# Kernel optimization log

Hardware: AMD Instinct MI355X
Metric: run time of the kernel (lower is better)

The kernel has to match this reference:

```python
import jax, jax.numpy as jnp
import numpy as np

B, D_IN, D, E = 65536, 512, 512, 8  # batch, input dim, node hidden dim, n_children (=decision dim)


def setup_inputs() -> dict:
    key = jax.random.key(0)
    ks = jax.random.split(key, 5)
    s = 0.02  # weight init scale
    return {
        "x": jax.random.normal(ks[0], (B, D_IN), jnp.float32),
        "W_root": jax.random.normal(ks[1], (D_IN, D), jnp.float32) * s,
        "b_root": jnp.zeros((D,), jnp.float32),
        "W_dec": jax.random.normal(ks[2], (D, E), jnp.float32) * s,
        "b_dec": jnp.zeros((E,), jnp.float32),
        "W_leaf": jax.random.normal(ks[3], (E, D, D), jnp.float32) * s,
        "b_leaf": jnp.zeros((E, D), jnp.float32),
        "W_ldec": jax.random.normal(ks[4], (E, D, E), jnp.float32) * s,
        "b_ldec": jnp.zeros((E, E), jnp.float32),
    }


def reference(x, W_root, b_root, W_dec, b_dec, W_leaf, b_leaf, W_ldec, b_ldec):
    # Root node (Dense+relu), flatten is a no-op on [B, D]
    h = jax.nn.relu(x @ W_root + b_root)                                 # [B, D]
    dec = jax.nn.softmax(h @ W_dec + b_dec, axis=-1)                     # [B, E] root decision (softmax, outputDim>1)
    route = jnp.argmax(dec, axis=-1)                                     # [B] hard routing
    # Leaf children: each leaf applies its own node Dense+relu and decision Dense+softmax.
    # Dense reference for the boolean-mask dispatch/combine: compute all experts on all
    # samples, then gather each sample's routed expert output (math-equivalent to the
    # original gather-per-mask + concat + reorder-gather, since partitions are disjoint).
    lh = jax.nn.relu(jnp.einsum('bd,edh->ebh', h, W_leaf) + b_leaf[:, None, :])     # [E, B, D]
    ldec = jax.nn.softmax(jnp.einsum('ebd,edo->ebo', lh, W_ldec) + b_ldec[:, None, :], axis=-1)  # [E, B, E]
    sel = jnp.take_along_axis(ldec.transpose(1, 0, 2), route[:, None, None], axis=1)[:, 0]  # [B, E]
    # concat root decisionOut [B,1,E] with ordered leaf outputs [B,1,E] along axis -2
    return jnp.concatenate([dec[:, None, :], sel[:, None, :]], axis=1)  # [B, 2, E]
```

## Files before the change

### kernel.cpp

```cpp
#include <hip/hip_runtime.h>
#include <stdint.h>

#define DD   512
#define EE   8

typedef __bf16 bf16x8 __attribute__((ext_vector_type(8)));
typedef float  f32x4  __attribute__((ext_vector_type(4)));

__device__ __forceinline__ unsigned short f2bf(float f) {
    union { float f; unsigned int i; } v; v.f = f;
    unsigned int x = v.i;
    x += 0x7fffu + ((x >> 16) & 1u);
    return (unsigned short)(x >> 16);
}
__device__ __forceinline__ void gload_lds16(const void* g, void* l) {
    __builtin_amdgcn_global_load_lds(
        (const __attribute__((address_space(1))) unsigned int*)g,
        (__attribute__((address_space(3))) unsigned int*)l, 16, 0, 0);
}
__device__ __forceinline__ f32x4 mfma_bf16(bf16x8 a, bf16x8 b, f32x4 c) {
    return __builtin_amdgcn_mfma_f32_16x16x32_bf16(a, b, c, 0, 0, 0);
}

__global__ __launch_bounds__(256) void k_wsplit(
    const float* __restrict__ W_root,
    unsigned short* __restrict__ WrTh, unsigned short* __restrict__ WrTl)
{
    __shared__ float tile[64][65];
    int tl = blockIdx.x, tr = tl >> 3, tc = tl & 7;
    int t = threadIdx.x;
    #pragma unroll
    for (int j = 0; j < 16; j++) {
        int i2 = t + j * 256; int r = i2 >> 6, c = i2 & 63;
        tile[r][c] = W_root[(size_t)(tr * 64 + r) * DD + tc * 64 + c];
    }
    __syncthreads();
    #pragma unroll
    for (int j = 0; j < 16; j++) {
        int i2 = t + j * 256; int r = i2 >> 6, c = i2 & 63;
        float v = tile[c][r];
        __bf16 hb = (__bf16)v;
        __bf16 lb = (__bf16)(v - (float)hb);
        size_t di = (size_t)(tc * 64 + r) * DD + tr * 64 + c;
        union { __bf16 b; unsigned short u; } uh, ul; uh.b = hb; ul.b = lb;
        WrTh[di] = uh.u; WrTl[di] = ul.u;
    }
}

__global__ __launch_bounds__(256) void k_trW(
    const float* __restrict__ W_leaf, unsigned short* __restrict__ WlT)
{
    __shared__ unsigned short tile[64][65];
    int bid = blockIdx.x;
    int e = bid >> 6;
    int tl = bid & 63, tr = tl >> 3, tc = tl & 7;
    const float* src = W_leaf + (size_t)e * DD * DD;
    unsigned short* dst = WlT + (size_t)e * DD * DD;
    int t = threadIdx.x;
    #pragma unroll
    for (int j = 0; j < 16; j++) {
        int i2 = t + j * 256; int r = i2 >> 6, c = i2 & 63;
        tile[r][c] = f2bf(src[(size_t)(tr * 64 + r) * DD + tc * 64 + c]);
    }
    __syncthreads();
    #pragma unroll
    for (int j = 0; j < 16; j++) {
        int i2 = t + j * 256; int r = i2 >> 6, c = i2 & 63;
        dst[(size_t)(tc * 64 + r) * DD + tr * 64 + c] = tile[c][r];
    }
}

__global__ __launch_bounds__(256) void k_trpad(
    const float* __restrict__ W_ldec, unsigned short* __restrict__ WldT)
{
    int idx = blockIdx.x * 256 + threadIdx.x;
    int e = idx >> 13, rem = idx & 8191;
    int o = rem >> 9, k = rem & 511;
    unsigned short v = 0;
    if (o < 8) v = f2bf(W_ldec[((size_t)e * DD + k) * EE + o]);
    WldT[idx] = v;
}

__global__ __launch_bounds__(256) void k_root(
    const float* __restrict__ x,
    const unsigned short* __restrict__ WrTh,
    const unsigned short* __restrict__ WrTl,
    const float* __restrict__ b_root,
    const float* __restrict__ W_dec,
    unsigned short* __restrict__ hbuf,
    float* __restrict__ logit_part)
{
    __shared__ unsigned short lsAh[128 * 32];
    __shared__ unsigned short lsAl[128 * 32];
    __shared__ unsigned short lsBh[128 * 32];
    __shared__ unsigned short lsBl[128 * 32];

    int bid = blockIdx.x;
    int mb = (bid >> 5) * 8 + (bid & 7);
    int cb = (bid >> 3) & 3;
    int m0 = mb * 128, n0 = cb * 128;

    int t = threadIdx.x;
    int wid = t >> 6, lane = t & 63;
    int wr = wid >> 1, wc = wid & 1;
    int l15 = lane & 15, l4 = lane >> 4;

    int ar = t >> 1, ah16 = (t & 1) * 16;
    const float* pA = x + (size_t)(m0 + ar) * DD + ah16;
    const unsigned short* srcBh0 = WrTh + (size_t)(n0 + (t >> 2)) * DD + (t & 3) * 8;
    const unsigned short* srcBh1 = srcBh0 + (size_t)64 * DD;
    const unsigned short* srcBl0 = WrTl + (size_t)(n0 + (t >> 2)) * DD + (t & 3) * 8;
    const unsigned short* srcBl1 = srcBl0 + (size_t)64 * DD;
    unsigned short* dBh0 = &lsBh[t * 8];
    unsigned short* dBh1 = &lsBh[2048 + t * 8];
    unsigned short* dBl0 = &lsBl[t * 8];
    unsigned short* dBl1 = &lsBl[2048 + t * 8];

    f32x4 acc[4][4];
    #pragma unroll
    for (int m = 0; m < 4; m++)
        #pragma unroll
        for (int n = 0; n < 4; n++) acc[m][n] = (f32x4){0.f, 0.f, 0.f, 0.f};

    for (int k0 = 0; k0 < DD; k0 += 32) {
        const float4* pAv = (const float4*)(pA + k0);
        float4 v0 = pAv[0], v1 = pAv[1], v2 = pAv[2], v3 = pAv[3];
        float vv[16] = {v0.x,v0.y,v0.z,v0.w, v1.x,v1.y,v1.z,v1.w,
                        v2.x,v2.y,v2.z,v2.w, v3.x,v3.y,v3.z,v3.w};
        bf16x8 hv0, hv1, lv0, lv1;
        #pragma unroll
        for (int j = 0; j < 8; j++) {
            __bf16 hb = (__bf16)vv[j];
            hv0[j] = hb; lv0[j] = (__bf16)(vv[j] - (float)hb);
        }
        #pragma unroll
        for (int j = 0; j < 8; j++) {
            __bf16 hb = (__bf16)vv[8 + j];
            hv1[j] = hb; lv1[j] = (__bf16)(vv[8 + j] - (float)hb);
        }
        __syncthreads();
        *(bf16x8*)&lsAh[ar * 32 + ah16]     = hv0;
        *(bf16x8*)&lsAh[ar * 32 + ah16 + 8] = hv1;
        *(bf16x8*)&lsAl[ar * 32 + ah16]     = lv0;
        *(bf16x8*)&lsAl[ar * 32 + ah16 + 8] = lv1;
        gload_lds16(srcBh0 + k0, dBh0);
        gload_lds16(srcBh1 + k0, dBh1);
        gload_lds16(srcBl0 + k0, dBl0);
        gload_lds16(srcBl1 + k0, dBl1);
        __syncthreads();

        bf16x8 fah[4], fal[4], fbh[4], fbl[4];
        #pragma unroll
        for (int m = 0; m < 4; m++) {
            int ro = (wr * 64 + m * 16 + l15) * 32 + l4 * 8;
            fah[m] = *(const bf16x8*)&lsAh[ro];
            fal[m] = *(const bf16x8*)&lsAl[ro];
        }
        #pragma unroll
        for (int n = 0; n < 4; n++) {
            int ro = (wc * 64 + n * 16 + l15) * 32 + l4 * 8;
            fbh[n] = *(const bf16x8*)&lsBh[ro];
            fbl[n] = *(const bf16x8*)&lsBl[ro];
        }
        #pragma unroll
        for (int m = 0; m < 4; m++)
            #pragma unroll
            for (int n = 0; n < 4; n++) {
                acc[m][n] = mfma_bf16(fah[m], fbh[n], acc[m][n]);
                acc[m][n] = mfma_bf16(fah[m], fbl[n], acc[m][n]);
                acc[m][n] = mfma_bf16(fal[m], fbh[n], acc[m][n]);
            }
    }

    float wdl[4][8], bcol[4];
    #pragma unroll
    for (int n = 0; n < 4; n++) {
        int colg = n0 + wc * 64 + n * 16 + l15;
        bcol[n] = b_root[colg];
        #pragma unroll
        for (int o = 0; o < 8; o++) wdl[n][o] = W_dec[colg * 8 + o];
    }
    int p = cb * 2 + wc;
    #pragma unroll
    for (int m = 0; m < 4; m++) {
        #pragma unroll
        for (int i = 0; i < 4; i++) {
            int rowg = m0 + wr * 64 + m * 16 + l4 * 4 + i;
            float s[8];
            #pragma unroll
            for (int o = 0; o < 8; o++) s[o] = 0.f;
            #pragma unroll
            for (int n = 0; n < 4; n++) {
                float v = acc[m][n][i] + bcol[n];
                v = fmaxf(v, 0.f);
                hbuf[(size_t)rowg * DD + (n0 + wc * 64 + n * 16 + l15)] = f2bf(v);
                #pragma unroll
                for (int o = 0; o < 8; o++) s[o] = fmaf(v, wdl[n][o], s[o]);
            }
            #pragma unroll
            for (int d = 1; d < 16; d <<= 1)
                #pragma unroll
                for (int o = 0; o < 8; o++) s[o] += __shfl_xor(s[o], d, 64);
            if (l15 == 0) {
                #pragma unroll
                for (int o = 0; o < 8; o++)
                    logit_part[((size_t)p * 65536 + rowg) * 8 + o] = s[o];
            }
        }
    }
}

__global__ __launch_bounds__(256) void k_dec(
    const float* __restrict__ logit_part,
    const float* __restrict__ b_dec,
    float* __restrict__ out,
    int* __restrict__ route,
    int* __restrict__ meta,
    int* __restrict__ rescue_list)
{
    int b = blockIdx.x * 256 + threadIdx.x;
    double lg[8];
    #pragma unroll
    for (int o = 0; o < 8; o++) lg[o] = (double)b_dec[o];
    for (int ppp = 0; ppp < 8; ppp++) {
        #pragma unroll
        for (int o = 0; o < 8; o++)
            lg[o] += (double)logit_part[((size_t)ppp * 65536 + b) * 8 + o];
    }
    double mx = -1e300, mx2 = -1e300; int idx = 0;
    #pragma unroll
    for (int o = 0; o < 8; o++) {
        if (lg[o] > mx) { mx2 = mx; mx = lg[o]; idx = o; }
        else if (lg[o] > mx2) mx2 = lg[o];
    }
    double ev[8], s = 0.0;
    #pragma unroll
    for (int o = 0; o < 8; o++) { ev[o] = exp(lg[o] - mx); s += ev[o]; }
    double inv = 1.0 / s;
    float4 o0, o1;
    o0.x = (float)(ev[0]*inv); o0.y = (float)(ev[1]*inv);
    o0.z = (float)(ev[2]*inv); o0.w = (float)(ev[3]*inv);
    o1.x = (float)(ev[4]*inv); o1.y = (float)(ev[5]*inv);
    o1.z = (float)(ev[6]*inv); o1.w = (float)(ev[7]*inv);
    float4* op = (float4*)(out + (size_t)b * 16);
    op[0] = o0; op[1] = o1;
    route[b] = idx;
    if (mx - mx2 < 1e-4) {
        int pos = atomicAdd(&meta[27], 1);
        if (pos < 8192) rescue_list[pos] = b;
    }
}

__global__ __launch_bounds__(256) void k_rescue(
    const float* __restrict__ x,
    const float* __restrict__ W_root,
    const float* __restrict__ b_root,
    const float* __restrict__ W_dec,
    const float* __restrict__ b_dec,
    const int* __restrict__ rescue_list,
    const int* __restrict__ meta,
    float* __restrict__ out,
    int* __restrict__ route)
{
    int nresc = min(meta[27], 8192);
    if ((int)blockIdx.x >= nresc) return;
    int row = rescue_list[blockIdx.x];
    int t = threadIdx.x;

    __shared__ float xr[512];
    __shared__ double red[4][8];
    xr[t * 2]     = x[(size_t)row * DD + t * 2];
    xr[t * 2 + 1] = x[(size_t)row * DD + t * 2 + 1];
    __syncthreads();

    int d0 = t, d1 = t + 256;
    double a0 = 0.0, a1 = 0.0;
    for (int k = 0; k < DD; k++) {
        double xv = (double)xr[k];
        a0 += xv * (double)W_root[(size_t)k * DD + d0];
        a1 += xv * (double)W_root[(size_t)k * DD + d1];
    }
    double h0 = fmax(a0 + (double)b_root[d0], 0.0);
    double h1 = fmax(a1 + (double)b_root[d1], 0.0);
    double so[8];
    #pragma unroll
    for (int o = 0; o < 8; o++)
        so[o] = h0 * (double)W_dec[d0 * 8 + o] + h1 * (double)W_dec[d1 * 8 + o];
    #pragma unroll
    for (int d = 1; d < 64; d <<= 1)
        #pragma unroll
        for (int o = 0; o < 8; o++) so[o] += __shfl_xor(so[o], d, 64);
    if ((t & 63) == 0) {
        #pragma unroll
        for (int o = 0; o < 8; o++) red[t >> 6][o] = so[o];
    }
    __syncthreads();
    if (t == 0) {
        double lg[8]; double mx = -1e300; int idx = 0;
        #pragma unroll
        for (int o = 0; o < 8; o++) {
            lg[o] = red[0][o] + red[1][o] + red[2][o] + red[3][o] + (double)b_dec[o];
            if (lg[o] > mx) { mx = lg[o]; idx = o; }
        }
        double ev[8], s = 0.0;
        #pragma unroll
        for (int o = 0; o < 8; o++) { ev[o] = exp(lg[o] - mx); s += ev[o]; }
        double inv = 1.0 / s;
        float4 o0, o1;
        o0.x = (float)(ev[0]*inv); o0.y = (float)(ev[1]*inv);
        o0.z = (float)(ev[2]*inv); o0.w = (float)(ev[3]*inv);
        o1.x = (float)(ev[4]*inv); o1.y = (float)(ev[5]*inv);
        o1.z = (float)(ev[6]*inv); o1.w = (float)(ev[7]*inv);
        float4* op = (float4*)(out + (size_t)row * 16);
        op[0] = o0; op[1] = o1;
        route[row] = idx;
    }
}

__global__ __launch_bounds__(256) void k_count(
    const int* __restrict__ route, int* __restrict__ meta)
{
    __shared__ int wcnt[4][8];
    int b = blockIdx.x * 256 + threadIdx.x;
    int e = route[b];
    int lane = threadIdx.x & 63, wv = threadIdx.x >> 6;
    #pragma unroll
    for (int ex = 0; ex < 8; ex++) {
        unsigned long long m = __ballot(e == ex);
        if (lane == 0) wcnt[wv][ex] = __popcll(m);
    }
    __syncthreads();
    if (threadIdx.x < 8) {
        int ex = threadIdx.x;
        atomicAdd(&meta[ex], wcnt[0][ex] + wcnt[1][ex] + wcnt[2][ex] + wcnt[3][ex]);
    }
}

__global__ void k_scan(int* __restrict__ meta)
{
    if (threadIdx.x == 0 && blockIdx.x == 0) {
        int run = 0, rb = 0;
        for (int e = 0; e < 8; e++) {
            int c = meta[e];
            meta[16 + e] = run;
            meta[8 + e]  = run;
            int n = (c + 127) >> 7;
            for (int j = 0; j < n; j++) meta[32 + rb + j] = e | (j << 8);
            rb += n;
            run += n << 7;
        }
        meta[24] = rb;
    }
}

__global__ __launch_bounds__(256) void k_scatter(
    const int* __restrict__ route, int* __restrict__ meta, int* __restrict__ rows_list)
{
    __shared__ int wcnt[4][8];
    __shared__ int wbase[4][8];
    int b = blockIdx.x * 256 + threadIdx.x;
    int e = route[b];
    int lane = threadIdx.x & 63, wv = threadIdx.x >> 6;
    unsigned long long mymask = 0;
    #pragma unroll
    for (int ex = 0; ex < 8; ex++) {
        unsigned long long m = __ballot(e == ex);
        if (e == ex) mymask = m;
        if (lane == 0) wcnt[wv][ex] = __popcll(m);
    }
    int myrank = __popcll(mymask & ((1ULL << lane) - 1ULL));
    __syncthreads();
    if (threadIdx.x < 8) {
        int ex = threadIdx.x;
        int c0 = wcnt[0][ex], c1 = wcnt[1][ex], c2 = wcnt[2][ex], c3 = wcnt[3][ex];
        int base = atomicAdd(&meta[8 + ex], c0 + c1 + c2 + c3);
        wbase[0][ex] = base;
        wbase[1][ex] = base + c0;
        wbase[2][ex] = base + c0 + c1;
        wbase[3][ex] = base + c0 + c1 + c2;
    }
    __syncthreads();
    rows_list[wbase[wv][e] + myrank] = b;
}

__global__ __launch_bounds__(256) void k_gemm2(
    const unsigned short* __restrict__ hbuf,
    const unsigned short* __restrict__ WlT,
    const float* __restrict__ b_leaf,
    const unsigned short* __restrict__ WldT,
    const int* __restrict__ rows_list,
    const int* __restrict__ meta,
    float* __restrict__ ldec_part)
{
    __shared__ unsigned short lsA[128 * 32];
    __shared__ unsigned short lsB[128 * 32];
    __shared__ unsigned short lh[128 * 136];

    int bid = blockIdx.x;
    int rbid = (bid >> 5) * 8 + (bid & 7);
    int cb = (bid >> 3) & 3;
    if (rbid >= meta[24]) return;
    int pk = meta[32 + rbid];
    int e = pk & 255, lrb = pk >> 8;
    int poff_e = meta[16 + e], cnt_e = meta[e];
    int n0 = cb * 128;

    int t = threadIdx.x;
    int wid = t >> 6, lane = t & 63;
    int wr = wid >> 1, wc = wid & 1;
    int l15 = lane & 15, l4 = lane >> 4;

    int slot0 = poff_e + lrb * 128 + (t >> 2);
    int slot1 = slot0 + 64;
    int lastv = poff_e + cnt_e - 1;
    int grow0 = rows_list[min(slot0, lastv)];
    int grow1 = rows_list[min(slot1, lastv)];
    const unsigned short* srcA0 = hbuf + (size_t)grow0 * DD + (t & 3) * 8;
    const unsigned short* srcA1 = hbuf + (size_t)grow1 * DD + (t & 3) * 8;
    const unsigned short* srcB0 = WlT + (size_t)e * DD * DD + (size_t)(n0 + (t >> 2)) * DD + (t & 3) * 8;
    const unsigned short* srcB1 = srcB0 + (size_t)64 * DD;
    unsigned short* dA0 = &lsA[t * 8];
    unsigned short* dA1 = &lsA[2048 + t * 8];
    unsigned short* dB0 = &lsB[t * 8];
    unsigned short* dB1 = &lsB[2048 + t * 8];

    f32x4 acc[4][4];
    #pragma unroll
    for (int m = 0; m < 4; m++)
        #pragma unroll
        for (int n = 0; n < 4; n++) acc[m][n] = (f32x4){0.f, 0.f, 0.f, 0.f};

    for (int k0 = 0; k0 < DD; k0 += 32) {
        __syncthreads();
        gload_lds16(srcA0 + k0, dA0);
        gload_lds16(srcA1 + k0, dA1);
        gload_lds16(srcB0 + k0, dB0);
        gload_lds16(srcB1 + k0, dB1);
        __syncthreads();
        bf16x8 af[4], bfr[4];
        #pragma unroll
        for (int m = 0; m < 4; m++)
            af[m] = *(const bf16x8*)&lsA[(wr * 64 + m * 16 + l15) * 32 + l4 * 8];
        #pragma unroll
        for (int n = 0; n < 4; n++)
            bfr[n] = *(const bf16x8*)&lsB[(wc * 64 + n * 16 + l15) * 32 + l4 * 8];
        #pragma unroll
        for (int m = 0; m < 4; m++)
            #pragma unroll
            for (int n = 0; n < 4; n++)
                acc[m][n] = mfma_bf16(af[m], bfr[n], acc[m][n]);
    }

    #pragma unroll
    for (int n = 0; n < 4; n++) {
        int coll = wc * 64 + n * 16 + l15;
        float bv = b_leaf[(size_t)e * DD + n0 + coll];
        #pragma unroll
        for (int m = 0; m < 4; m++) {
            int rl = wr * 64 + m * 16 + l4 * 4;
            #pragma unroll
            for (int i = 0; i < 4; i++) {
                float v = acc[m][n][i] + bv;
                v = v > 0.f ? v : 0.f;
                lh[(rl + i) * 136 + coll] = f2bf(v);
            }
        }
    }
    __syncthreads();

    f32x4 acc2[2];
    acc2[0] = (f32x4){0.f, 0.f, 0.f, 0.f};
    acc2[1] = (f32x4){0.f, 0.f, 0.f, 0.f};
    #pragma unroll
    for (int kk = 0; kk < 4; kk++) {
        bf16x8 bb = *(const bf16x8*)(WldT + ((size_t)e * 16 + l15) * DD + n0 + kk * 32 + l4 * 8);
        #pragma unroll
        for (int m2 = 0; m2 < 2; m2++) {
            bf16x8 aa = *(const bf16x8*)&lh[(wid * 32 + m2 * 16 + l15) * 136 + kk * 32 + l4 * 8];
            acc2[m2] = mfma_bf16(aa, bb, acc2[m2]);
        }
    }
    if (l15 < 8) {
        #pragma unroll
        for (int m2 = 0; m2 < 2; m2++)
            #pragma unroll
            for (int i = 0; i < 4; i++) {
                int rl = wid * 32 + m2 * 16 + l4 * 4 + i;
                int s = min(poff_e + lrb * 128 + rl, lastv);
                int brow = rows_list[s];
                ldec_part[((size_t)cb * 65536 + brow) * 8 + l15] = acc2[m2][i];
            }
    }
}

__global__ __launch_bounds__(256) void k_sel(
    const float* __restrict__ ldec_part,
    const int* __restrict__ route,
    const float* __restrict__ b_ldec,
    float* __restrict__ out)
{
    int b = blockIdx.x * 256 + threadIdx.x;
    int e = route[b];
    float lg[8];
    #pragma unroll
    for (int o = 0; o < 8; o++) lg[o] = b_ldec[e * 8 + o];
    #pragma unroll
    for (int p = 0; p < 4; p++) {
        const float4* ap = (const float4*)(ldec_part + ((size_t)p * 65536 + b) * 8);
        float4 a0 = ap[0], a1 = ap[1];
        lg[0]+=a0.x; lg[1]+=a0.y; lg[2]+=a0.z; lg[3]+=a0.w;
        lg[4]+=a1.x; lg[5]+=a1.y; lg[6]+=a1.z; lg[7]+=a1.w;
    }
    float mx = -1e30f;
    #pragma unroll
    for (int o = 0; o < 8; o++) mx = fmaxf(mx, lg[o]);
    float ev[8], s = 0.f;
    #pragma unroll
    for (int o = 0; o < 8; o++) { ev[o] = expf(lg[o] - mx); s += ev[o]; }
    float inv = 1.f / s;
    float4 o0, o1;
    o0.x = ev[0]*inv; o0.y = ev[1]*inv; o0.z = ev[2]*inv; o0.w = ev[3]*inv;
    o1.x = ev[4]*inv; o1.y = ev[5]*inv; o1.z = ev[6]*inv; o1.w = ev[7]*inv;
    float4* op = (float4*)(out + (size_t)b * 16 + 8);
    op[0] = o0; op[1] = o1;
}

extern "C" void kernel_launch(void* const* d_in, const int* in_sizes, int n_in,
                              void* d_out, int out_size, void* d_ws, size_t ws_size,
                              hipStream_t stream)
{
    const float* x      = (const float*)d_in[0];
    const float* W_root = (const float*)d_in[1];
    const float* b_root = (const float*)d_in[2];
    const float* W_dec  = (const float*)d_in[3];
    const float* b_dec  = (const float*)d_in[4];
    const float* W_leaf = (const float*)d_in[5];
    const float* b_leaf = (const float*)d_in[6];
    const float* W_ldec = (const float*)d_in[7];
    const float* b_ldec = (const float*)d_in[8];
    float* out = (float*)d_out;

    char* w = (char*)d_ws;
    unsigned short* hbuf       = (unsigned short*)(w);
    float*          logit_part = (float*)(w + 67108864);
    unsigned short* WlT        = (unsigned short*)(w + 83886080);
    unsigned short* WldT       = (unsigned short*)(w + 88080384);
    float*          ldec_part  = (float*)(w + 88211456);
    int*            route      = (int*)(w + 96600064);
    int*            rows_list  = (int*)(w + 96862208);
    int*            meta       = (int*)(w + 97128448);
    unsigned short* WrTh       = (unsigned short*)(w + 97132544);
    unsigned short* WrTl       = (unsigned short*)(w + 97656832);
    int*            rescue     = (int*)(w + 98181120);
    const size_t WS_NEED = 98213888ULL;
    if (ws_size < WS_NEED) return;

    hipMemsetAsync(meta, 0, 4096, stream);

    k_wsplit <<<64,   256, 0, stream>>>(W_root, WrTh, WrTl);
    k_trW    <<<512,  256, 0, stream>>>(W_leaf, WlT);
    k_trpad  <<<256,  256, 0, stream>>>(W_ldec, WldT);
    k_root   <<<2048, 256, 0, stream>>>(x, WrTh, WrTl, b_root, W_dec, hbuf, logit_part);
    k_dec    <<<256,  256, 0, stream>>>(logit_part, b_dec, out, route, meta, rescue);
    k_rescue <<<8192, 256, 0, stream>>>(x, W_root, b_root, W_dec, b_dec, rescue, meta, out, route);
    k_count  <<<256,  256, 0, stream>>>(route, meta);
    k_scan   <<<1,    64,  0, stream>>>(meta);
    k_scatter<<<256,  256, 0, stream>>>(route, meta, rows_list);
    k_gemm2  <<<2080, 256, 0, stream>>>(hbuf, WlT, b_leaf, WldT, rows_list, meta, ldec_part);
    k_sel    <<<256,  256, 0, stream>>>(ldec_part, route, b_ldec, out);
}
```

Before: 290.2 us.

## Drop split-bf16 root GEMM, compute root logits via MFMA from staged LDS tile

The root GEMM now runs as a single bf16 MFMA pass instead of three hi/lo compensated passes, and the W_root low-part buffer is removed. To offset the lost precision, the near-tie rescue threshold is widened so more ambiguous rows get recomputed in fp32 by the rescue kernel. The epilogue stages the relu'd bf16 tile in LDS, writes hbuf with coalesced vector stores, and computes the decision logits with a small MFMA against a transposed padded W_dec. This replaces the per-lane FMA and shuffle reduction, and halves the logit partials from 8 to 4. Softmax in k_dec moves from double to float exp. Routing correctness now leans more on the rescue path, and the rescue count is capped at 8192.

```diff
diff --git a/kernel.cpp b/kernel.cpp
--- a/kernel.cpp
+++ b/kernel.cpp
@@ -6,6 +6,7 @@
 
 typedef __bf16 bf16x8 __attribute__((ext_vector_type(8)));
 typedef float  f32x4  __attribute__((ext_vector_type(4)));
+typedef unsigned short u16x8 __attribute__((ext_vector_type(8)));
 
 __device__ __forceinline__ unsigned short f2bf(float f) {
     union { float f; unsigned int i; } v; v.f = f;
@@ -22,28 +23,22 @@
     return __builtin_amdgcn_mfma_f32_16x16x32_bf16(a, b, c, 0, 0, 0);
 }
 
-__global__ __launch_bounds__(256) void k_wsplit(
-    const float* __restrict__ W_root,
-    unsigned short* __restrict__ WrTh, unsigned short* __restrict__ WrTl)
-{
-    __shared__ float tile[64][65];
+__global__ __launch_bounds__(256) void k_wtr(
+    const float* __restrict__ W_root, unsigned short* __restrict__ WrTh)
+{
+    __shared__ unsigned short tile[64][65];
     int tl = blockIdx.x, tr = tl >> 3, tc = tl & 7;
     int t = threadIdx.x;
     #pragma unroll
     for (int j = 0; j < 16; j++) {
         int i2 = t + j * 256; int r = i2 >> 6, c = i2 & 63;
-        tile[r][c] = W_root[(size_t)(tr * 64 + r) * DD + tc * 64 + c];
+        tile[r][c] = f2bf(W_root[(size_t)(tr * 64 + r) * DD + tc * 64 + c]);
     }
     __syncthreads();
     #pragma unroll
     for (int j = 0; j < 16; j++) {
         int i2 = t + j * 256; int r = i2 >> 6, c = i2 & 63;
-        float v = tile[c][r];
-        __bf16 hb = (__bf16)v;
-        __bf16 lb = (__bf16)(v - (float)hb);
-        size_t di = (size_t)(tc * 64 + r) * DD + tr * 64 + c;
-        union { __bf16 b; unsigned short u; } uh, ul; uh.b = hb; ul.b = lb;
-        WrTh[di] = uh.u; WrTl[di] = ul.u;
+        WrTh[(size_t)(tc * 64 + r) * DD + tr * 64 + c] = tile[c][r];
     }
 }
 
@@ -81,19 +76,25 @@
     WldT[idx] = v;
 }
 
+__global__ __launch_bounds__(256) void k_trdec(
+    const float* __restrict__ W_dec, unsigned short* __restrict__ WdT)
+{
+    int idx = blockIdx.x * 256 + threadIdx.x;
+    int o = idx >> 9, k = idx & 511;
+    WdT[idx] = (o < 8) ? f2bf(W_dec[(size_t)k * EE + o]) : (unsigned short)0;
+}
+
 __global__ __launch_bounds__(256) void k_root(
     const float* __restrict__ x,
     const unsigned short* __restrict__ WrTh,
-    const unsigned short* __restrict__ WrTl,
     const float* __restrict__ b_root,
-    const float* __restrict__ W_dec,
+    const unsigned short* __restrict__ WdT,
     unsigned short* __restrict__ hbuf,
     float* __restrict__ logit_part)
 {
-    __shared__ unsigned short lsAh[128 * 32];
-    __shared__ unsigned short lsAl[128 * 32];
-    __shared__ unsigned short lsBh[128 * 32];
-    __shared__ unsigned short lsBl[128 * 32];
+    __shared__ unsigned short smem[128 * 136];
+    unsigned short* lsA = smem;
+    unsigned short* lsB = smem + 4096;
 
     int bid = blockIdx.x;
     int mb = (bid >> 5) * 8 + (bid & 7);
@@ -107,14 +108,10 @@
 
     int ar = t >> 1, ah16 = (t & 1) * 16;
     const float* pA = x + (size_t)(m0 + ar) * DD + ah16;
-    const unsigned short* srcBh0 = WrTh + (size_t)(n0 + (t >> 2)) * DD + (t & 3) * 8;
-    const unsigned short* srcBh1 = srcBh0 + (size_t)64 * DD;
-    const unsigned short* srcBl0 = WrTl + (size_t)(n0 + (t >> 2)) * DD + (t & 3) * 8;
-    const unsigned short* srcBl1 = srcBl0 + (size_t)64 * DD;
-    unsigned short* dBh0 = &lsBh[t * 8];
-    unsigned short* dBh1 = &lsBh[2048 + t * 8];
-    unsigned short* dBl0 = &lsBl[t * 8];
-    unsigned short* dBl1 = &lsBl[2048 + t * 8];
+    const unsigned short* srcB0 = WrTh + (size_t)(n0 + (t >> 2)) * DD + (t & 3) * 8;
+    const unsigned short* srcB1 = srcB0 + (size_t)64 * DD;
+    unsigned short* dB0 = &lsB[t * 8];
+    unsigned short* dB1 = &lsB[2048 + t * 8];
 
     f32x4 acc[4][4];
     #pragma unroll
@@ -127,86 +124,78 @@
         float4 v0 = pAv[0], v1 = pAv[1], v2 = pAv[2], v3 = pAv[3];
         float vv[16] = {v0.x,v0.y,v0.z,v0.w, v1.x,v1.y,v1.z,v1.w,
                         v2.x,v2.y,v2.z,v2.w, v3.x,v3.y,v3.z,v3.w};
-        bf16x8 hv0, hv1, lv0, lv1;
-        #pragma unroll
-        for (int j = 0; j < 8; j++) {
-            __bf16 hb = (__bf16)vv[j];
-            hv0[j] = hb; lv0[j] = (__bf16)(vv[j] - (float)hb);
-        }
-        #pragma unroll
-        for (int j = 0; j < 8; j++) {
-            __bf16 hb = (__bf16)vv[8 + j];
-            hv1[j] = hb; lv1[j] = (__bf16)(vv[8 + j] - (float)hb);
-        }
+        bf16x8 hv0, hv1;
+        #pragma unroll
+        for (int j = 0; j < 8; j++) { hv0[j] = (__bf16)vv[j]; hv1[j] = (__bf16)vv[8 + j]; }
         __syncthreads();
-        *(bf16x8*)&lsAh[ar * 32 + ah16]     = hv0;
-        *(bf16x8*)&lsAh[ar * 32 + ah16 + 8] = hv1;
-        *(bf16x8*)&lsAl[ar * 32 + ah16]     = lv0;
-        *(bf16x8*)&lsAl[ar * 32 + ah16 + 8] = lv1;
-        gload_lds16(srcBh0 + k0, dBh0);
-        gload_lds16(srcBh1 + k0, dBh1);
-        gload_lds16(srcBl0 + k0, dBl0);
-        gload_lds16(srcBl1 + k0, dBl1);
+        *(bf16x8*)&lsA[ar * 32 + ah16]     = hv0;
+        *(bf16x8*)&lsA[ar * 32 + ah16 + 8] = hv1;
+        gload_lds16(srcB0 + k0, dB0);
+        gload_lds16(srcB1 + k0, dB1);
         __syncthreads();
 
-        bf16x8 fah[4], fal[4], fbh[4], fbl[4];
-        #pragma unroll
-        for (int m = 0; m < 4; m++) {
-            int ro = (wr * 64 + m * 16 + l15) * 32 + l4 * 8;
-            fah[m] = *(const bf16x8*)&lsAh[ro];
-            fal[m] = *(const bf16x8*)&lsAl[ro];
-        }
-        #pragma unroll
-        for (int n = 0; n < 4; n++) {
-            int ro = (wc * 64 + n * 16 + l15) * 32 + l4 * 8;
-            fbh[n] = *(const bf16x8*)&lsBh[ro];
-            fbl[n] = *(const bf16x8*)&lsBl[ro];
-        }
+        bf16x8 fa[4], fb[4];
+        #pragma unroll
+        for (int m = 0; m < 4; m++)
+            fa[m] = *(const bf16x8*)&lsA[(wr * 64 + m * 16 + l15) * 32 + l4 * 8];
+        #pragma unroll
+        for (int n = 0; n < 4; n++)
+            fb[n] = *(const bf16x8*)&lsB[(wc * 64 + n * 16 + l15) * 32 + l4 * 8];
         #pragma unroll
         for (int m = 0; m < 4; m++)
             #pragma unroll
-            for (int n = 0; n < 4; n++) {
-                acc[m][n] = mfma_bf16(fah[m], fbh[n], acc[m][n]);
-                acc[m][n] = mfma_bf16(fah[m], fbl[n], acc[m][n]);
-                acc[m][n] = mfma_bf16(fal[m], fbh[n], acc[m][n]);
-            }
-    }
-
-    float wdl[4][8], bcol[4];
+            for (int n = 0; n < 4; n++)
+                acc[m][n] = mfma_bf16(fa[m], fb[n], acc[m][n]);
+    }
+    __syncthreads();
+
+    float bcol[4];
+    #pragma unroll
+    for (int n = 0; n < 4; n++) bcol[n] = b_root[n0 + wc * 64 + n * 16 + l15];
     #pragma unroll
     for (int n = 0; n < 4; n++) {
-        int colg = n0 + wc * 64 + n * 16 + l15;
-        bcol[n] = b_root[colg];
-        #pragma unroll
-        for (int o = 0; o < 8; o++) wdl[n][o] = W_dec[colg * 8 + o];
-    }
-    int p = cb * 2 + wc;
-    #pragma unroll
-    for (int m = 0; m < 4; m++) {
-        #pragma unroll
-        for (int i = 0; i < 4; i++) {
-            int rowg = m0 + wr * 64 + m * 16 + l4 * 4 + i;
-            float s[8];
+        int coll = wc * 64 + n * 16 + l15;
+        #pragma unroll
+        for (int m = 0; m < 4; m++) {
+            int rl = wr * 64 + m * 16 + l4 * 4;
             #pragma unroll
-            for (int o = 0; o < 8; o++) s[o] = 0.f;
-            #pragma unroll
-            for (int n = 0; n < 4; n++) {
+            for (int i = 0; i < 4; i++) {
                 float v = acc[m][n][i] + bcol[n];
-                v = fmaxf(v, 0.f);
-                hbuf[(size_t)rowg * DD + (n0 + wc * 64 + n * 16 + l15)] = f2bf(v);
-                #pragma unroll
-                for (int o = 0; o < 8; o++) s[o] = fmaf(v, wdl[n][o], s[o]);
-            }
-            #pragma unroll
-            for (int d = 1; d < 16; d <<= 1)
-                #pragma unroll
-                for (int o = 0; o < 8; o++) s[o] += __shfl_xor(s[o], d, 64);
-            if (l15 == 0) {
-                #pragma unroll
-                for (int o = 0; o < 8; o++)
-                    logit_part[((size_t)p * 65536 + rowg) * 8 + o] = s[o];
+                v = v > 0.f ? v : 0.f;
+                smem[(rl + i) * 136 + coll] = f2bf(v);
             }
         }
+    }
+    __syncthreads();
+
+    {
+        int r = t >> 1, c0 = (t & 1) * 64;
+        unsigned short* dst = hbuf + (size_t)(m0 + r) * DD + n0 + c0;
+        #pragma unroll
+        for (int j = 0; j < 8; j++)
+            *(u16x8*)(dst + j * 8) = *(const u16x8*)&smem[r * 136 + c0 + j * 8];
+    }
+
+    f32x4 acc2[2];
+    acc2[0] = (f32x4){0.f, 0.f, 0.f, 0.f};
+    acc2[1] = (f32x4){0.f, 0.f, 0.f, 0.f};
+    #pragma unroll
+    for (int kk = 0; kk < 4; kk++) {
+        bf16x8 bb = *(const bf16x8*)(WdT + (size_t)l15 * DD + n0 + kk * 32 + l4 * 8);
+        #pragma unroll
+        for (int m2 = 0; m2 < 2; m2++) {
+            bf16x8 aa = *(const bf16x8*)&smem[(wid * 32 + m2 * 16 + l15) * 136 + kk * 32 + l4 * 8];
+            acc2[m2] = mfma_bf16(aa, bb, acc2[m2]);
+        }
+    }
+    if (l15 < 8) {
+        #pragma unroll
+        for (int m2 = 0; m2 < 2; m2++)
+            #pragma unroll
+            for (int i = 0; i < 4; i++) {
+                int rowg = m0 + wid * 32 + m2 * 16 + l4 * 4 + i;
+                logit_part[((size_t)cb * 65536 + rowg) * 8 + l15] = acc2[m2][i];
+            }
     }
 }
 
@@ -222,7 +211,8 @@
     double lg[8];
     #pragma unroll
     for (int o = 0; o < 8; o++) lg[o] = (double)b_dec[o];
-    for (int ppp = 0; ppp < 8; ppp++) {
+    #pragma unroll
+    for (int ppp = 0; ppp < 4; ppp++) {
         #pragma unroll
         for (int o = 0; o < 8; o++)
             lg[o] += (double)logit_part[((size_t)ppp * 65536 + b) * 8 + o];
@@ -233,19 +223,17 @@
         if (lg[o] > mx) { mx2 = mx; mx = lg[o]; idx = o; }
         else if (lg[o] > mx2) mx2 = lg[o];
     }
-    double ev[8], s = 0.0;
-    #pragma unroll
-    for (int o = 0; o < 8; o++) { ev[o] = exp(lg[o] - mx); s += ev[o]; }
-    double inv = 1.0 / s;
+    float ev[8], s = 0.f;
+    #pragma unroll
+    for (int o = 0; o < 8; o++) { ev[o] = expf((float)(lg[o] - mx)); s += ev[o]; }
+    float inv = 1.f / s;
     float4 o0, o1;
-    o0.x = (float)(ev[0]*inv); o0.y = (float)(ev[1]*inv);
-    o0.z = (float)(ev[2]*inv); o0.w = (float)(ev[3]*inv);
-    o1.x = (float)(ev[4]*inv); o1.y = (float)(ev[5]*inv);
-    o1.z = (float)(ev[6]*inv); o1.w = (float)(ev[7]*inv);
+    o0.x = ev[0]*inv; o0.y = ev[1]*inv; o0.z = ev[2]*inv; o0.w = ev[3]*inv;
+    o1.x = ev[4]*inv; o1.y = ev[5]*inv; o1.z = ev[6]*inv; o1.w = ev[7]*inv;
     float4* op = (float4*)(out + (size_t)b * 16);
     op[0] = o0; op[1] = o1;
     route[b] = idx;
-    if (mx - mx2 < 1e-4) {
+    if (mx - mx2 < 3e-3) {
         int pos = atomicAdd(&meta[27], 1);
         if (pos < 8192) rescue_list[pos] = b;
     }
@@ -543,24 +531,25 @@
     char* w = (char*)d_ws;
     unsigned short* hbuf       = (unsigned short*)(w);
     float*          logit_part = (float*)(w + 67108864);
-    unsigned short* WlT        = (unsigned short*)(w + 83886080);
-    unsigned short* WldT       = (unsigned short*)(w + 88080384);
-    float*          ldec_part  = (float*)(w + 88211456);
-    int*            route      = (int*)(w + 96600064);
-    int*            rows_list  = (int*)(w + 96862208);
-    int*            meta       = (int*)(w + 97128448);
-    unsigned short* WrTh       = (unsigned short*)(w + 97132544);
-    unsigned short* WrTl       = (unsigned short*)(w + 97656832);
-    int*            rescue     = (int*)(w + 98181120);
-    const size_t WS_NEED = 98213888ULL;
+    unsigned short* WlT        = (unsigned short*)(w + 75497472);
+    unsigned short* WldT       = (unsigned short*)(w + 79691776);
+    unsigned short* WdT        = (unsigned short*)(w + 79822848);
+    float*          ldec_part  = (float*)(w + 79839232);
+    int*            route      = (int*)(w + 88227840);
+    int*            rows_list  = (int*)(w + 88489984);
+    unsigned short* WrTh       = (unsigned short*)(w + 88756224);
+    int*            rescue     = (int*)(w + 89280512);
+    int*            meta       = (int*)(w + 89313280);
+    const size_t WS_NEED = 89317376ULL;
     if (ws_size < WS_NEED) return;
 
     hipMemsetAsync(meta, 0, 4096, stream);
 
-    k_wsplit <<<64,   256, 0, stream>>>(W_root, WrTh, WrTl);
+    k_wtr    <<<64,   256, 0, stream>>>(W_root, WrTh);
     k_trW    <<<512,  256, 0, stream>>>(W_leaf, WlT);
     k_trpad  <<<256,  256, 0, stream>>>(W_ldec, WldT);
-    k_root   <<<2048, 256, 0, stream>>>(x, WrTh, WrTl, b_root, W_dec, hbuf, logit_part);
+    k_trdec  <<<32,   256, 0, stream>>>(W_dec, WdT);
+    k_root   <<<2048, 256, 0, stream>>>(x, WrTh, b_root, WdT, hbuf, logit_part);
     k_dec    <<<256,  256, 0, stream>>>(logit_part, b_dec, out, route, meta, rescue);
     k_rescue <<<8192, 256, 0, stream>>>(x, W_root, b_root, W_dec, b_dec, rescue, meta, out, route);
     k_count  <<<256,  256, 0, stream>>>(route, meta);
```

Result: faster. 275.3 us (-5.1%).
